# Kernel tuning notes

Hardware: AMD Instinct MI355X
Metric: run time of the kernel (lower is better)

## Reference

```python
import jax, jax.numpy as jnp
from jax import lax
import numpy as np

N = 4
ALPHA_AP = 0.85
ALPHA_DS = 0.1
ALPHA_LR = 1.0
C1 = 0.01 ** 2
C2 = 0.03 ** 2


def resize_ac(img, nh, nw):
    # bilinear resize, align_corners=True (matches F.interpolate(..., align_corners=True))
    B, C, H, W = img.shape
    ys = jnp.linspace(0.0, H - 1.0, nh)
    xs = jnp.linspace(0.0, W - 1.0, nw)
    y0 = jnp.floor(ys).astype(jnp.int32)
    y1 = jnp.minimum(y0 + 1, H - 1)
    x0 = jnp.floor(xs).astype(jnp.int32)
    x1 = jnp.minimum(x0 + 1, W - 1)
    wy = (ys - y0).astype(img.dtype)[None, None, :, None]
    wx = (xs - x0).astype(img.dtype)[None, None, None, :]
    top = img[:, :, y0, :] * (1.0 - wy) + img[:, :, y1, :] * wy
    return top[:, :, :, x0] * (1.0 - wx) + top[:, :, :, x1] * wx


def build_pyramid(img):
    B, C, H, W = img.shape
    pyr = [img]
    for i in range(N - 1):
        r = 2 ** (i + 1)
        pyr.append(resize_ac(pyr[i], H // r, W // r))  # resize previous level, as in torch code
    return pyr


def x_grad(img):
    # replicate-pad right then diff -> last column is exactly zero
    g = img[:, :, :, :-1] - img[:, :, :, 1:]
    return jnp.concatenate([g, jnp.zeros_like(img[:, :, :, :1])], axis=3)


def y_grad(img):
    g = img[:, :, :-1, :] - img[:, :, 1:, :]
    return jnp.concatenate([g, jnp.zeros_like(img[:, :, :1, :])], axis=2)


def avgpool3(x):
    # AvgPool2d(3, 1), VALID padding
    return lax.reduce_window(x, 0.0, lax.add, (1, 1, 3, 3), (1, 1, 1, 1), 'VALID') / 9.0


def grid_sample_zeros(img, gx, gy):
    # bilinear grid_sample, padding_mode='zeros', align_corners=True
    B, C, H, W = img.shape
    x = (gx + 1.0) * 0.5 * (W - 1)
    y = (gy + 1.0) * 0.5 * (H - 1)
    x0 = jnp.floor(x)
    y0 = jnp.floor(y)

    def corner(xi, yi, w):
        valid = (xi >= 0) & (xi <= W - 1) & (yi >= 0) & (yi <= H - 1)
        xc = jnp.clip(xi, 0, W - 1).astype(jnp.int32)
        yc = jnp.clip(yi, 0, H - 1).astype(jnp.int32)
        vals = jax.vmap(lambda im, yy, xx: im[:, yy, xx])(img, yc, xc)  # [B,C,H,W]
        return vals * (w * valid.astype(img.dtype))[:, None]

    return (corner(x0, y0, (x0 + 1 - x) * (y0 + 1 - y))
            + corner(x0 + 1, y0, (x - x0) * (y0 + 1 - y))
            + corner(x0, y0 + 1, (x0 + 1 - x) * (y - y0))
            + corner(x0 + 1, y0 + 1, (x - x0) * (y - y0)))


def apply_disparity(img, disp):
    # standard Monodepth bilinear sampler: shift x_base in [0,1] by disp, grid_sample
    B, C, H, W = img.shape
    x_base = jnp.linspace(0.0, 1.0, W)[None, None, :]
    y_base = jnp.linspace(0.0, 1.0, H)[None, :, None]
    gx = 2.0 * (x_base + disp[:, 0]) - 1.0  # [B,H,W]
    gy = jnp.broadcast_to(2.0 * y_base - 1.0, gx.shape)
    return grid_sample_zeros(img, gx, gy)


def dssim(x, y):
    mu_x = avgpool3(x)
    mu_y = avgpool3(y)
    sig_x = avgpool3(x * x) - mu_x ** 2
    sig_y = avgpool3(y * y) - mu_y ** 2
    cov = avgpool3(x * y) - mu_x * mu_y
    ssim = ((2.0 * mu_x * mu_y + C1) * (2.0 * cov + C2)) / ((mu_x ** 2 + mu_y ** 2 + C1) * (sig_x + sig_y + C2))
    return jnp.mean(jnp.clip((1.0 - ssim) / 2.0, 0.0, 1.0))


def smoothness(disp, img, level):
    wx = jnp.exp(-jnp.mean(jnp.abs(x_grad(img)), axis=1, keepdims=True))
    wy = jnp.exp(-jnp.mean(jnp.abs(y_grad(img)), axis=1, keepdims=True))
    sx = x_grad(disp) * wx
    sy = y_grad(disp) * wy
    return jnp.mean(jnp.abs(sx) + jnp.abs(sy)) / (2 ** level)


def loss_forward(disps, left, right):
    lp = build_pyramid(left)
    rp = build_pyramid(right)
    dl = [d[:, 0:1] for d in disps]
    dr = [d[:, 1:2] for d in disps]
    left_est = [apply_disparity(rp[i], -dl[i]) for i in range(N)]
    right_est = [apply_disparity(lp[i], dr[i]) for i in range(N)]
    r2l_disp = [apply_disparity(dr[i], -dl[i]) for i in range(N)]
    l2r_disp = [apply_disparity(dl[i], dr[i]) for i in range(N)]
    # appearance matching (note: outer *ALPHA_AP matches the original's AP_loss*self.alpha_AP)
    AP = sum(ALPHA_AP * dssim(lp[i], left_est[i]) + (1.0 - ALPHA_AP) * jnp.mean(jnp.abs(lp[i] - left_est[i])) for i in range(N))
    AP = AP + sum(ALPHA_AP * dssim(rp[i], right_est[i]) + (1.0 - ALPHA_AP) * jnp.mean(jnp.abs(rp[i] - right_est[i])) for i in range(N))
    AP = AP * ALPHA_AP
    LR = sum(jnp.mean(jnp.abs(dl[i] - r2l_disp[i])) for i in range(N))
    LR = (LR + sum(jnp.mean(jnp.abs(dr[i] - l2r_disp[i])) for i in range(N))) * ALPHA_LR
    DS = sum(smoothness(dl[i], lp[i], i) for i in range(N))
    DS = (DS + sum(smoothness(dr[i], rp[i], i) for i in range(N))) * ALPHA_DS
    total = AP + LR + DS
    return total, AP, LR, DS


def setup_inputs() -> dict:
    key = jax.random.key(0)
    ks = jax.random.split(key, 6)
    B, H, W = 32, 256, 512
    inp = {}
    for i in range(N):
        h, w = H >> i, W >> i
        # normalized disparities in [0, 0.05) as in trained Monodepth
        inp[f'disp{i}'] = jax.random.uniform(ks[i], (B, 2, h, w), jnp.float32) * 0.05
    inp['left'] = jax.random.uniform(ks[4], (B, 3, H, W), jnp.float32)
    inp['right'] = jax.random.uniform(ks[5], (B, 3, H, W), jnp.float32)
    return inp


def reference(disp0, disp1, disp2, disp3, left, right):
    return loss_forward([disp0, disp1, disp2, disp3], left, right)
```

## Files before the change

kernel.cpp:

```cpp
#include <hip/hip_runtime.h>

#define BDIM 256
#define GRID 1024
#define W0C 512
#define H0C 256

struct LevelDesc {
    const float* lp; const float* rp; const float* dp;
    int H, W, nCW, nChunks, base, nPerSide;
};
struct Params {
    LevelDesc lv[4];
    double* acc; unsigned int* cnt; float* out;
};
struct PyrParams {
    const float* left; const float* right;
    float* l1; float* r1; float* l2; float* r2; float* l3; float* r3;
    double* acc; unsigned int* cnt;
};

#define E1 3145728LL
#define E2 786432LL
#define E3 196608LL
#define T1 (E1 / 2)

__device__ __forceinline__ float samp1(const float* __restrict__ src, int j, int i) {
    const float sy = 255.0f / 127.0f;
    const float sx = 511.0f / 255.0f;
    float y = fminf(j * sy, 255.0f);
    float x = fminf(i * sx, 511.0f);
    int y0 = (int)y, x0 = (int)x;
    int y1 = min(y0 + 1, 255), x1 = min(x0 + 1, 511);
    float wy = y - (float)y0, wx = x - (float)x0;
    const float* r0 = src + (long long)y0 * W0C;
    const float* r1 = src + (long long)y1 * W0C;
    float t0 = r0[x0] * (1.0f - wy) + r1[x0] * wy;
    float t1 = r0[x1] * (1.0f - wy) + r1[x1] * wy;
    return t0 * (1.0f - wx) + t1 * wx;
}

__global__ void __launch_bounds__(BDIM)
pyr1_kernel(PyrParams Q) {
    if (blockIdx.x == 0) {
        if (threadIdx.x < 32) Q.acc[threadIdx.x] = 0.0;
        else if (threadIdx.x == 32) *Q.cnt = 0u;
    }
    long long idx = (long long)blockIdx.x * BDIM + threadIdx.x;
    int side = idx >= T1;
    long long id = side ? idx - T1 : idx;
    int i2 = (int)(id & 127), j = (int)((id >> 7) & 127), bc = (int)(id >> 14);
    const float* src = (side ? Q.right : Q.left) + (long long)bc * (H0C * W0C);
    float2 o;
    o.x = samp1(src, j, 2 * i2);
    o.y = samp1(src, j, 2 * i2 + 1);
    ((float2*)(side ? Q.r1 : Q.l1))[id] = o;
}

__device__ __forceinline__ void taps1(int i, int Dd, int Ds, int* idx, float* w) {
    float s = (float)(Ds - 1) / (float)(Dd - 1);
    float p = fminf(i * s, (float)(Ds - 1));
    int a = (int)p; float t = p - (float)a;
    idx[0] = a; w[0] = 1.0f - t;
    idx[1] = min(a + 1, Ds - 1); w[1] = t;
}
__device__ __forceinline__ void taps2(int i, int D2, int D1, int D0, int* idx, float* w) {
    int i1[2]; float w1[2];
    taps1(i, D2, D1, i1, w1);
#pragma unroll
    for (int k = 0; k < 2; ++k) {
        int t[2]; float u[2];
        taps1(i1[k], D1, D0, t, u);
        idx[2 * k] = t[0];     w[2 * k] = w1[k] * u[0];
        idx[2 * k + 1] = t[1]; w[2 * k + 1] = w1[k] * u[1];
    }
}

__global__ void __launch_bounds__(BDIM)
pyr23_kernel(PyrParams Q) {
    long long idx = (long long)blockIdx.x * BDIM + threadIdx.x;
    if (idx < 2 * E2) {
        int side = idx >= E2;
        long long id = side ? idx - E2 : idx;
        int i = (int)(id & 127), j = (int)((id >> 7) & 63), bc = (int)(id >> 13);
        const float* src = (side ? Q.r1 : Q.l1) + (long long)bc * (128 * 256);
        int yi[2], xi[2]; float yw[2], xw[2];
        taps1(j, 64, 128, yi, yw);
        taps1(i, 128, 256, xi, xw);
        float a = 0.0f;
#pragma unroll
        for (int u = 0; u < 2; ++u) {
            const float* row = src + (long long)yi[u] * 256;
            a = fmaf(yw[u], fmaf(xw[0], row[xi[0]], xw[1] * row[xi[1]]), a);
        }
        (side ? Q.r2 : Q.l2)[id] = a;
    } else {
        long long r = idx - 2 * E2;
        int side = r >= E3;
        long long id = side ? r - E3 : r;
        int i = (int)(id & 63), j = (int)((id >> 6) & 31), bc = (int)(id >> 11);
        const float* src = (side ? Q.r1 : Q.l1) + (long long)bc * (128 * 256);
        int yi[4], xi[4]; float yw[4], xw[4];
        taps2(j, 32, 64, 128, yi, yw);
        taps2(i, 64, 128, 256, xi, xw);
        float a = 0.0f;
#pragma unroll
        for (int u = 0; u < 4; ++u) {
            const float* row = src + (long long)yi[u] * 256;
            float s = 0.0f;
#pragma unroll
            for (int v = 0; v < 4; ++v) s = fmaf(xw[v], row[xi[v]], s);
            a = fmaf(yw[u], s, a);
        }
        (side ? Q.r3 : Q.l3)[id] = a;
    }
}

__device__ __forceinline__ float ssim_term(float Sx, float Sy, float Sxx, float Syy, float Sxy) {
    const float C1v = 0.0001f;
    const float C2v = 0.0009f;
    float mux = Sx * (1.0f / 9.0f), muy = Sy * (1.0f / 9.0f);
    float sigx = Sxx * (1.0f / 9.0f) - mux * mux;
    float sigy = Syy * (1.0f / 9.0f) - muy * muy;
    float cov  = Sxy * (1.0f / 9.0f) - mux * muy;
    float num = (2.0f * mux * muy + C1v) * (2.0f * cov + C2v);
    float den = (mux * mux + muy * muy + C1v) * (sigx + sigy + C2v);
    float v = (1.0f - num * __builtin_amdgcn_rcpf(den)) * 0.5f;
    return fminf(fmaxf(v, 0.0f), 1.0f);
}

__device__ void finalize_dev(double* __restrict__ acc, float* __restrict__ out) {
    const int B = 32;
    double AP = 0.0, LR = 0.0, DS = 0.0;
    for (int i = 0; i < 4; ++i) {
        int h = H0C >> i, w = W0C >> i;
        double nss = (double)B * 3.0 * (double)(h - 2) * (double)(w - 2);
        double nl1 = (double)B * 3.0 * (double)h * (double)w;
        double nd  = (double)B * (double)h * (double)w;
        double ssl = atomicAdd(acc + 0 + i, 0.0)  + atomicAdd(acc + 4 + i, 0.0);
        double l1l = atomicAdd(acc + 8 + i, 0.0)  + atomicAdd(acc + 12 + i, 0.0);
        double lrl = atomicAdd(acc + 16 + i, 0.0) + atomicAdd(acc + 20 + i, 0.0);
        double dsl = atomicAdd(acc + 24 + i, 0.0) + atomicAdd(acc + 28 + i, 0.0);
        AP += 0.85 * (ssl / nss) + 0.15 * (l1l / nl1);
        LR += lrl / nd;
        DS += (dsl / nd) / (double)(1 << i);
    }
    AP *= 0.85;
    DS *= 0.1;
    out[0] = (float)(AP + LR + DS);
    out[1] = (float)AP;
    out[2] = (float)LR;
    out[3] = (float)DS;
}

__global__ void __launch_bounds__(BDIM)
mega_kernel(Params P) {
    const int lane = threadIdx.x & 63;
    const int wid  = threadIdx.x >> 6;
    const int w    = blockIdx.x * (BDIM / 64) + wid;

    int level = 0;
    if (w >= P.lv[1].base) level = 1;
    if (w >= P.lv[2].base) level = 2;
    if (w >= P.lv[3].base) level = 3;
    LevelDesc L;
    if (level == 0) L = P.lv[0];
    else if (level == 1) L = P.lv[1];
    else if (level == 2) L = P.lv[2];
    else L = P.lv[3];

    int rel = w - L.base;
    const int side = (rel >= L.nPerSide) ? 1 : 0;
    rel -= side * L.nPerSide;
    const int chunk = rel % L.nChunks;
    const int r3i = rel / L.nChunks;
    const int cw = r3i % L.nCW;
    const int b  = r3i / L.nCW;

    const int H = L.H, W = L.W;
    const long long HW = (long long)H * W;
    const float Wm1f = (float)(W - 1);
    const float sgn = side ? 1.0f : -1.0f;

    const float* xim = (side ? L.rp : L.lp) + (long long)b * 3 * HW;
    const float* sim = (side ? L.lp : L.rp) + (long long)b * 3 * HW;
    const float* dme = L.dp + (long long)b * 2 * HW + (side ? HW : 0);
    const float* dot = L.dp + (long long)b * 2 * HW + (side ? 0 : HW);

    const int base = cw * 126;
    const int c0 = base + 2 * lane;
    const int c1 = c0 + 1;
    const bool in0 = c0 < W, in1 = c1 < W;
    const int cc = min(c0, W - 2) >> 1;
    const float fc0 = (float)c0, fc1 = (float)c1;

    const bool lastW = (cw == L.nCW - 1);
    const bool own0 = in0 && (c0 < base + 126 || lastW);
    const bool own1 = in1 && (c1 < base + 126 || lastW);
    const bool ownS0 = own0 && (c0 <= W - 3);
    const bool ownS1 = own1 && (c1 <= W - 3);

    const int r0 = (chunk * H) / L.nChunks;
    const int r1 = ((chunk + 1) * H) / L.nChunks;
    const int jend = min(r1 + 1, H - 1);

    float Pst[3][5][2], Lst[3][5][2];
#pragma unroll
    for (int c = 0; c < 3; ++c)
#pragma unroll
        for (int s = 0; s < 5; ++s) { Pst[c][s][0] = 0.f; Pst[c][s][1] = 0.f;
                                      Lst[c][s][0] = 0.f; Lst[c][s][1] = 0.f; }
    float pd0 = 0.f, pd1 = 0.f;
    float pxv[3][2] = {{0.f,0.f},{0.f,0.f},{0.f,0.f}};

    float f_ss = 0.f, f_l1 = 0.f, f_lr = 0.f, f_ds = 0.f;

    for (int j = r0; j <= jend; ++j) {
        const long long ro = (long long)j * W;
        float2 dpair = ((const float2*)(dme + ro))[cc];
        float d0 = dpair.x, d1 = dpair.y;

        float xq0 = fmaf(sgn * d0, Wm1f, fc0);
        float xq1 = fmaf(sgn * d1, Wm1f, fc1);
        float xf0 = floorf(xq0), xf1 = floorf(xq1);
        int g0 = (int)xf0, g1 = (int)xf1;
        float t0 = xq0 - xf0, t1 = xq1 - xf1;
        float w00 = (g0 >= 0 && g0 < W)      ? 1.0f - t0 : 0.0f;
        float w01 = (g0 >= -1 && g0 < W - 1) ? t0        : 0.0f;
        float w10 = (g1 >= 0 && g1 < W)      ? 1.0f - t1 : 0.0f;
        float w11 = (g1 >= -1 && g1 < W - 1) ? t1        : 0.0f;
        int a0 = min(max(g0, 0), W - 1);
        int a1 = min(max(g0 + 1, 0), W - 1);
        int b0 = min(max(g1, 0), W - 1);
        int b1 = min(max(g1 + 1, 0), W - 1);

        const float* dor = dot + ro;
        float wv0 = dor[a0] * w00 + dor[a1] * w01;
        float wv1 = dor[b0] * w10 + dor[b1] * w11;

        float xv[3][2], yv[3][2];
#pragma unroll
        for (int c = 0; c < 3; ++c) {
            const float* xr = xim + (long long)c * HW + ro;
            const float* sr = sim + (long long)c * HW + ro;
            float2 xp2 = ((const float2*)xr)[cc];
            xv[c][0] = in0 ? xp2.x : 0.f;
            xv[c][1] = in1 ? xp2.y : 0.f;
            yv[c][0] = sr[a0] * w00 + sr[a1] * w01;
            yv[c][1] = sr[b0] * w10 + sr[b1] * w11;
            if (!in0) yv[c][0] = 0.f;
            if (!in1) yv[c][1] = 0.f;
        }

        const bool rowOwn = j < r1;
        if (rowOwn) {
            if (own0) {
                f_l1 += fabsf(xv[0][0] - yv[0][0]) + fabsf(xv[1][0] - yv[1][0]) + fabsf(xv[2][0] - yv[2][0]);
                f_lr += fabsf(d0 - wv0);
            }
            if (own1) {
                f_l1 += fabsf(xv[0][1] - yv[0][1]) + fabsf(xv[1][1] - yv[1][1]) + fabsf(xv[2][1] - yv[2][1]);
                f_lr += fabsf(d1 - wv1);
            }
        }

        {
            float dn  = __shfl_down(d0, 1);
            float xn0 = __shfl_down(xv[0][0], 1);
            float xn1 = __shfl_down(xv[1][0], 1);
            float xn2 = __shfl_down(xv[2][0], 1);
            if (rowOwn) {
                if (own0 && c0 < W - 1) {
                    float g = fabsf(xv[0][0] - xv[0][1]) + fabsf(xv[1][0] - xv[1][1]) + fabsf(xv[2][0] - xv[2][1]);
                    f_ds += fabsf((d0 - d1) * __expf(-g * (1.0f / 3.0f)));
                }
                if (own1 && c1 < W - 1) {
                    float g = fabsf(xv[0][1] - xn0) + fabsf(xv[1][1] - xn1) + fabsf(xv[2][1] - xn2);
                    f_ds += fabsf((d1 - dn) * __expf(-g * (1.0f / 3.0f)));
                }
            }
        }
        if (j > r0 && (j - 1) < r1) {
            if (own0) {
                float g = fabsf(pxv[0][0] - xv[0][0]) + fabsf(pxv[1][0] - xv[1][0]) + fabsf(pxv[2][0] - xv[2][0]);
                f_ds += fabsf((pd0 - d0) * __expf(-g * (1.0f / 3.0f)));
            }
            if (own1) {
                float g = fabsf(pxv[0][1] - xv[0][1]) + fabsf(pxv[1][1] - xv[1][1]) + fabsf(pxv[2][1] - xv[2][1]);
                f_ds += fabsf((pd1 - d1) * __expf(-g * (1.0f / 3.0f)));
            }
        }
        pd0 = d0; pd1 = d1;
#pragma unroll
        for (int c = 0; c < 3; ++c) { pxv[c][0] = xv[c][0]; pxv[c][1] = xv[c][1]; }

        const bool emit = (j >= r0 + 2);
#pragma unroll
        for (int c = 0; c < 3; ++c) {
            float cs[5][2];
#pragma unroll
            for (int p = 0; p < 2; ++p) {
                float cx = xv[c][p], cy = yv[c][p];
                float v5[5] = {cx, cy, cx * cx, cy * cy, cx * cy};
#pragma unroll
                for (int s = 0; s < 5; ++s) {
                    cs[s][p] = Pst[c][s][p] + v5[s];
                    Pst[c][s][p] = Lst[c][s][p] + v5[s];
                    Lst[c][s][p] = v5[s];
                }
            }
            if (emit) {
                float w0s[5], w1s[5];
#pragma unroll
                for (int s = 0; s < 5; ++s) {
                    float n0 = __shfl_down(cs[s][0], 1);
                    float n1 = __shfl_down(cs[s][1], 1);
                    w0s[s] = cs[s][0] + cs[s][1] + n0;
                    w1s[s] = cs[s][1] + n0 + n1;
                }
                float ts0 = ssim_term(w0s[0], w0s[1], w0s[2], w0s[3], w0s[4]);
                float ts1 = ssim_term(w1s[0], w1s[1], w1s[2], w1s[3], w1s[4]);
                f_ss += (ownS0 ? ts0 : 0.f) + (ownS1 ? ts1 : 0.f);
            }
        }
    }

#pragma unroll
    for (int o = 32; o > 0; o >>= 1) {
        f_ss += __shfl_down(f_ss, o);
        f_l1 += __shfl_down(f_l1, o);
        f_lr += __shfl_down(f_lr, o);
        f_ds += __shfl_down(f_ds, o);
    }
    __shared__ float red[BDIM / 64][4];
    __shared__ int meta[3];
    if (threadIdx.x == 0) { meta[0] = level; meta[1] = side; }
    if (lane == 0) {
        red[wid][0] = f_ss; red[wid][1] = f_l1;
        red[wid][2] = f_lr; red[wid][3] = f_ds;
    }
    __syncthreads();
    if (threadIdx.x < 4) {
        int t = threadIdx.x;
        double s = (double)red[0][t] + (double)red[1][t]
                 + (double)red[2][t] + (double)red[3][t];
        atomicAdd(P.acc + t * 8 + meta[1] * 4 + meta[0], s);
    }
    __syncthreads();
    if (threadIdx.x == 0) {
        __threadfence();
        unsigned int old = atomicAdd(P.cnt, 1u);
        meta[2] = (old == (unsigned int)(gridDim.x - 1)) ? 1 : 0;
    }
    __syncthreads();
    if (meta[2] && threadIdx.x == 0) {
        __threadfence();
        finalize_dev(P.acc, P.out);
    }
}

extern "C" void kernel_launch(void* const* d_in, const int* in_sizes, int n_in,
                              void* d_out, int out_size, void* d_ws, size_t ws_size,
                              hipStream_t stream) {
    const float* dsp[4];
    for (int i = 0; i < 4; ++i) dsp[i] = (const float*)d_in[i];
    const float* left  = (const float*)d_in[4];
    const float* right = (const float*)d_in[5];

    double* acc = (double*)d_ws;
    unsigned int* cnt = (unsigned int*)((char*)d_ws + 256);
    float* buf = (float*)((char*)d_ws + 512);

    PyrParams Q;
    Q.left = left; Q.right = right; Q.acc = acc; Q.cnt = cnt;
    float* cur = buf;
    Q.l1 = cur; cur += E1;
    Q.r1 = cur; cur += E1;
    Q.l2 = cur; cur += E2;
    Q.r2 = cur; cur += E2;
    Q.l3 = cur; cur += E3;
    Q.r3 = cur; cur += E3;

    Params P;
    P.acc = acc; P.cnt = cnt; P.out = (float*)d_out;
    P.lv[0] = { left,  right, dsp[0], 256, 512, 5, 9,    0, 1440 };
    P.lv[1] = { Q.l1,  Q.r1,  dsp[1], 128, 256, 3, 5, 2880,  480 };
    P.lv[2] = { Q.l2,  Q.r2,  dsp[2],  64, 128, 1, 3, 3840,   96 };
    P.lv[3] = { Q.l3,  Q.r3,  dsp[3],  32,  64, 1, 1, 4032,   32 };

    pyr1_kernel<<<(int)(2 * T1 / BDIM), BDIM, 0, stream>>>(Q);
    pyr23_kernel<<<(int)(2 * (E2 + E3) / BDIM), BDIM, 0, stream>>>(Q);
    mega_kernel<<<GRID, BDIM, 0, stream>>>(P);
}
```

Baseline: 347.0 us.

## Fuse pyramid levels into one kernel sampling full-res source, and double row chunks

Merges the two pyramid kernels into a single launch. Levels 2 and 3 are now computed straight from the full-resolution images using composed separable bilinear taps (4x4 and 8x8), which removes the dependency on level 1 and one kernel launch but adds extra gathers per output. The main kernel's row chunk counts are doubled and the grid enlarged to 2064 blocks for more parallelism. The next row's disparity pair is now prefetched one iteration ahead. The risks are more redundant reads in the pyramid stage and extra halo rows from the finer chunking.

```diff
diff --git a/kernel.cpp b/kernel.cpp
--- a/kernel.cpp
+++ b/kernel.cpp
@@ -1,7 +1,7 @@
 #include <hip/hip_runtime.h>
 
 #define BDIM 256
-#define GRID 1024
+#define GRID 2064
 #define W0C 512
 #define H0C 256
 
@@ -23,6 +23,31 @@
 #define E2 786432LL
 #define E3 196608LL
 #define T1 (E1 / 2)
+#define TOTPYR (2 * (T1 + E2 + E3))
+
+__device__ __forceinline__ void taps1(int i, int Dd, int Ds, int* idx, float* w) {
+    float s = (float)(Ds - 1) / (float)(Dd - 1);
+    float p = fminf(i * s, (float)(Ds - 1));
+    int a = (int)p; float t = p - (float)a;
+    idx[0] = a; w[0] = 1.0f - t;
+    idx[1] = min(a + 1, Ds - 1); w[1] = t;
+}
+template<int NMAX>
+__device__ __forceinline__ int expand(int n, int Dd, int Ds, int* idx, float* w) {
+    int ti[NMAX]; float tw[NMAX];
+#pragma unroll
+    for (int k = 0; k < NMAX / 2; ++k) {
+        if (k < n) {
+            int t[2]; float u[2];
+            taps1(idx[k], Dd, Ds, t, u);
+            ti[2 * k] = t[0];     tw[2 * k] = w[k] * u[0];
+            ti[2 * k + 1] = t[1]; tw[2 * k + 1] = w[k] * u[1];
+        }
+    }
+#pragma unroll
+    for (int k = 0; k < NMAX; ++k) if (k < 2 * n) { idx[k] = ti[k]; w[k] = tw[k]; }
+    return 2 * n;
+}
 
 __device__ __forceinline__ float samp1(const float* __restrict__ src, int j, int i) {
     const float sy = 255.0f / 127.0f;
@@ -39,79 +64,68 @@
     return t0 * (1.0f - wx) + t1 * wx;
 }
 
+template<int N>
+__device__ __forceinline__ float sep_sample(const float* __restrict__ src,
+                                            const int* yi, const float* yw,
+                                            const int* xi, const float* xw) {
+    float acc = 0.0f;
+#pragma unroll
+    for (int u = 0; u < N; ++u) {
+        const float* row = src + (long long)yi[u] * W0C;
+        float s = 0.0f;
+#pragma unroll
+        for (int v = 0; v < N; ++v) s = fmaf(xw[v], row[xi[v]], s);
+        acc = fmaf(yw[u], s, acc);
+    }
+    return acc;
+}
+
 __global__ void __launch_bounds__(BDIM)
-pyr1_kernel(PyrParams Q) {
+pyramid_kernel(PyrParams Q) {
     if (blockIdx.x == 0) {
         if (threadIdx.x < 32) Q.acc[threadIdx.x] = 0.0;
         else if (threadIdx.x == 32) *Q.cnt = 0u;
     }
     long long idx = (long long)blockIdx.x * BDIM + threadIdx.x;
-    int side = idx >= T1;
-    long long id = side ? idx - T1 : idx;
-    int i2 = (int)(id & 127), j = (int)((id >> 7) & 127), bc = (int)(id >> 14);
-    const float* src = (side ? Q.right : Q.left) + (long long)bc * (H0C * W0C);
-    float2 o;
-    o.x = samp1(src, j, 2 * i2);
-    o.y = samp1(src, j, 2 * i2 + 1);
-    ((float2*)(side ? Q.r1 : Q.l1))[id] = o;
-}
-
-__device__ __forceinline__ void taps1(int i, int Dd, int Ds, int* idx, float* w) {
-    float s = (float)(Ds - 1) / (float)(Dd - 1);
-    float p = fminf(i * s, (float)(Ds - 1));
-    int a = (int)p; float t = p - (float)a;
-    idx[0] = a; w[0] = 1.0f - t;
-    idx[1] = min(a + 1, Ds - 1); w[1] = t;
-}
-__device__ __forceinline__ void taps2(int i, int D2, int D1, int D0, int* idx, float* w) {
-    int i1[2]; float w1[2];
-    taps1(i, D2, D1, i1, w1);
-#pragma unroll
-    for (int k = 0; k < 2; ++k) {
-        int t[2]; float u[2];
-        taps1(i1[k], D1, D0, t, u);
-        idx[2 * k] = t[0];     w[2 * k] = w1[k] * u[0];
-        idx[2 * k + 1] = t[1]; w[2 * k + 1] = w1[k] * u[1];
-    }
-}
-
-__global__ void __launch_bounds__(BDIM)
-pyr23_kernel(PyrParams Q) {
-    long long idx = (long long)blockIdx.x * BDIM + threadIdx.x;
-    if (idx < 2 * E2) {
-        int side = idx >= E2;
-        long long id = side ? idx - E2 : idx;
+    if (idx < 2 * T1) {
+        int side = idx >= T1;
+        long long id = side ? idx - T1 : idx;
+        int i2 = (int)(id & 127), j = (int)((id >> 7) & 127), bc = (int)(id >> 14);
+        const float* src = (side ? Q.right : Q.left) + (long long)bc * (H0C * W0C);
+        float2 o;
+        o.x = samp1(src, j, 2 * i2);
+        o.y = samp1(src, j, 2 * i2 + 1);
+        ((float2*)(side ? Q.r1 : Q.l1))[id] = o;
+    } else if (idx < 2 * T1 + 2 * E2) {
+        long long r = idx - 2 * T1;
+        int side = r >= E2;
+        long long id = side ? r - E2 : r;
         int i = (int)(id & 127), j = (int)((id >> 7) & 63), bc = (int)(id >> 13);
-        const float* src = (side ? Q.r1 : Q.l1) + (long long)bc * (128 * 256);
-        int yi[2], xi[2]; float yw[2], xw[2];
-        taps1(j, 64, 128, yi, yw);
-        taps1(i, 128, 256, xi, xw);
-        float a = 0.0f;
-#pragma unroll
-        for (int u = 0; u < 2; ++u) {
-            const float* row = src + (long long)yi[u] * 256;
-            a = fmaf(yw[u], fmaf(xw[0], row[xi[0]], xw[1] * row[xi[1]]), a);
-        }
-        (side ? Q.r2 : Q.l2)[id] = a;
+        const float* src = (side ? Q.right : Q.left) + (long long)bc * (H0C * W0C);
+        int yi[4], xi[4]; float yw[4], xw[4];
+        int ny = 1; yi[0] = j; yw[0] = 1.0f;
+        ny = expand<4>(ny, 64, 128, yi, yw);
+        ny = expand<4>(ny, 128, 256, yi, yw);
+        int nx = 1; xi[0] = i; xw[0] = 1.0f;
+        nx = expand<4>(nx, 128, 256, xi, xw);
+        nx = expand<4>(nx, 256, 512, xi, xw);
+        (side ? Q.r2 : Q.l2)[id] = sep_sample<4>(src, yi, yw, xi, xw);
     } else {
-        long long r = idx - 2 * E2;
+        long long r = idx - 2 * T1 - 2 * E2;
         int side = r >= E3;
         long long id = side ? r - E3 : r;
         int i = (int)(id & 63), j = (int)((id >> 6) & 31), bc = (int)(id >> 11);
-        const float* src = (side ? Q.r1 : Q.l1) + (long long)bc * (128 * 256);
-        int yi[4], xi[4]; float yw[4], xw[4];
-        taps2(j, 32, 64, 128, yi, yw);
-        taps2(i, 64, 128, 256, xi, xw);
-        float a = 0.0f;
-#pragma unroll
-        for (int u = 0; u < 4; ++u) {
-            const float* row = src + (long long)yi[u] * 256;
-            float s = 0.0f;
-#pragma unroll
-            for (int v = 0; v < 4; ++v) s = fmaf(xw[v], row[xi[v]], s);
-            a = fmaf(yw[u], s, a);
-        }
-        (side ? Q.r3 : Q.l3)[id] = a;
+        const float* src = (side ? Q.right : Q.left) + (long long)bc * (H0C * W0C);
+        int yi[8], xi[8]; float yw[8], xw[8];
+        int ny = 1; yi[0] = j; yw[0] = 1.0f;
+        ny = expand<8>(ny, 32, 64, yi, yw);
+        ny = expand<8>(ny, 64, 128, yi, yw);
+        ny = expand<8>(ny, 128, 256, yi, yw);
+        int nx = 1; xi[0] = i; xw[0] = 1.0f;
+        nx = expand<8>(nx, 64, 128, xi, xw);
+        nx = expand<8>(nx, 128, 256, xi, xw);
+        nx = expand<8>(nx, 256, 512, xi, xw);
+        (side ? Q.r3 : Q.l3)[id] = sep_sample<8>(src, yi, yw, xi, xw);
     }
 }
 
@@ -214,9 +228,12 @@
 
     float f_ss = 0.f, f_l1 = 0.f, f_lr = 0.f, f_ds = 0.f;
 
+    float2 dnx = ((const float2*)(dme + (long long)r0 * W))[cc];
+
     for (int j = r0; j <= jend; ++j) {
         const long long ro = (long long)j * W;
-        float2 dpair = ((const float2*)(dme + ro))[cc];
+        float2 dpair = dnx;
+        if (j < jend) dnx = ((const float2*)(dme + (long long)(j + 1) * W))[cc];
         float d0 = dpair.x, d1 = dpair.y;
 
         float xq0 = fmaf(sgn * d0, Wm1f, fc0);
@@ -382,12 +399,11 @@
 
     Params P;
     P.acc = acc; P.cnt = cnt; P.out = (float*)d_out;
-    P.lv[0] = { left,  right, dsp[0], 256, 512, 5, 9,    0, 1440 };
-    P.lv[1] = { Q.l1,  Q.r1,  dsp[1], 128, 256, 3, 5, 2880,  480 };
-    P.lv[2] = { Q.l2,  Q.r2,  dsp[2],  64, 128, 1, 3, 3840,   96 };
-    P.lv[3] = { Q.l3,  Q.r3,  dsp[3],  32,  64, 1, 1, 4032,   32 };
-
-    pyr1_kernel<<<(int)(2 * T1 / BDIM), BDIM, 0, stream>>>(Q);
-    pyr23_kernel<<<(int)(2 * (E2 + E3) / BDIM), BDIM, 0, stream>>>(Q);
+    P.lv[0] = { left,  right, dsp[0], 256, 512, 5, 18,    0, 2880 };
+    P.lv[1] = { Q.l1,  Q.r1,  dsp[1], 128, 256, 3, 10, 5760,  960 };
+    P.lv[2] = { Q.l2,  Q.r2,  dsp[2],  64, 128, 1,  6, 7680,  192 };
+    P.lv[3] = { Q.l3,  Q.r3,  dsp[3],  32,  64, 1,  3, 8064,   96 };
+
+    pyramid_kernel<<<(int)(TOTPYR / BDIM), BDIM, 0, stream>>>(Q);
     mega_kernel<<<GRID, BDIM, 0, stream>>>(P);
 }
```

Result: slower. 396.0 us (+14.1%).
